# Kernel optimization log

Measured on AMD Instinct MI355X. Metric: run time of the kernel, lower is better.

## Reference

```python
import jax, jax.numpy as jnp
import numpy as np

H, HKV, D, HID = 32, 8, 128, 4096
EPS = 1e-6
ROPE_BASE = 10000.0
SCALE = D ** -0.5


def setup_inputs() -> dict:
    key = jax.random.key(0)
    ks = jax.random.split(key, 4)
    T = 2048
    x = jax.random.normal(ks[0], (T, HID), dtype=jnp.float32)
    w_qkv = jax.random.normal(ks[1], ((H + 2 * HKV) * D, HID), dtype=jnp.float32) * (HID ** -0.5)
    b_qkv = jax.random.normal(ks[2], ((H + 2 * HKV) * D,), dtype=jnp.float32) * 0.02
    q_norm_w = jnp.ones((D,), dtype=jnp.float32)
    k_norm_w = jnp.ones((D,), dtype=jnp.float32)
    w_o = jax.random.normal(ks[3], (HID, H * D), dtype=jnp.float32) * ((H * D) ** -0.5)
    return {"x": x, "w_qkv": w_qkv, "b_qkv": b_qkv, "q_norm_w": q_norm_w,
            "k_norm_w": k_norm_w, "w_o": w_o}


def _rms_norm(t, w):
    # per-head RMSNorm over the last (head_dim) axis
    var = jnp.mean(t * t, axis=-1, keepdims=True)
    return t * jax.lax.rsqrt(var + EPS) * w


def _rope(t, cos, sin):
    # neox-style half rotation; cos/sin: [T, D//2], t: [T, h, D]
    t1, t2 = jnp.split(t, 2, axis=-1)
    c = cos[:, None, :]
    s = sin[:, None, :]
    return jnp.concatenate([t1 * c - t2 * s, t2 * c + t1 * s], axis=-1)


def reference(x, w_qkv, b_qkv, q_norm_w, k_norm_w, w_o):
    T = x.shape[0]
    qkv = x @ w_qkv.T + b_qkv                      # [T, (H+2*HKV)*D]
    q, k, v = jnp.split(qkv, [H * D, (H + HKV) * D], axis=-1)
    q = q.reshape(T, H, D)
    k = k.reshape(T, HKV, D)
    v = v.reshape(T, HKV, D)

    # QK RMSNorm
    q = _rms_norm(q, q_norm_w)
    k = _rms_norm(k, k_norm_w)

    # rotary embedding, base 10000, full head_dim
    pos = jnp.arange(T, dtype=jnp.float32)
    inv_freq = 1.0 / (ROPE_BASE ** (jnp.arange(0, D, 2, dtype=jnp.float32) / D))
    freqs = pos[:, None] * inv_freq[None, :]        # [T, D//2]
    cos, sin = jnp.cos(freqs), jnp.sin(freqs)
    q = _rope(q, cos, sin)
    k = _rope(k, cos, sin)

    # GQA: kv_head_mapping = arange(HKV).repeat_interleave(H // HKV)
    groups = H // HKV
    k = jnp.repeat(k, groups, axis=1)               # [T, H, D]
    v = jnp.repeat(v, groups, axis=1)

    scores = jnp.einsum('thd,shd->hts', q, k) * SCALE   # [H, T, T]
    causal = jnp.tril(jnp.ones((T, T), dtype=bool))
    scores = jnp.where(causal[None], scores, jnp.finfo(scores.dtype).min)
    probs = jax.nn.softmax(scores, axis=-1)
    out = jnp.einsum('hts,shd->thd', probs, v)      # [T, H, D]
    return out.reshape(T, H * D) @ w_o.T            # [T, HID]
```

## Files before the change

kernel.cpp:

```cpp
#include <hip/hip_runtime.h>
#include <stdint.h>
#include <stddef.h>

typedef __bf16 bf16_t;
typedef __bf16 bf16x8 __attribute__((ext_vector_type(8)));
typedef float  f32x4  __attribute__((ext_vector_type(4)));
typedef float  f32x8  __attribute__((ext_vector_type(8)));

#define T_SEQ 2048
#define NH    32
#define NKV   8
#define DH    128
#define HIDN  4096
#define NQKV  6144
#define SCALE 0.08838834764831845f
#define MBOUND 11.5f

__device__ inline float b2f(bf16_t v) {
  uint32_t u = ((uint32_t)__builtin_bit_cast(uint16_t, v)) << 16;
  return __builtin_bit_cast(float, u);
}
__device__ inline bf16_t f2b(float f) { return (bf16_t)f; }
__device__ inline void gl_lds16(const void* g, void* l) {
  __builtin_amdgcn_global_load_lds(
      (__attribute__((address_space(1))) void*)g,
      (__attribute__((address_space(3))) void*)l, 16, 0, 0);
}
__device__ inline f32x4 mfma16(bf16x8 a, bf16x8 b, f32x4 c) {
  return __builtin_amdgcn_mfma_f32_16x16x32_bf16(a, b, c, 0, 0, 0);
}
__device__ inline void store_val(float* p, float v)  { *p = v; }
__device__ inline void store_val(bf16_t* p, float v) { *p = f2b(v); }

template <typename T> struct Pack8;
template <> struct Pack8<bf16_t> { using type = bf16x8; };
template <> struct Pack8<float>  { using type = f32x8; };
__device__ inline bf16x8 to_bf8(bf16x8 v) { return v; }
__device__ inline bf16x8 to_bf8(f32x8 v) {
  bf16x8 o;
#pragma unroll
  for (int e = 0; e < 8; ++e) o[e] = f2b(v[e]);
  return o;
}

template <bool BIAS, typename TA, typename TB, typename TOUT>
__global__ __launch_bounds__(256)
void gemm_bt(const TA* __restrict__ A, const TB* __restrict__ Bw,
             const float* __restrict__ bias, TOUT* __restrict__ C,
             int M, int N, int K) {
  __shared__ __align__(16) char smem[32768];
  char* sA = smem;
  char* sB = smem + 16384;
  const int tid  = threadIdx.x;
  const int lane = tid & 63, wave = tid >> 6;
  const int quad = lane >> 4, l16 = lane & 15;
  const int wm = wave >> 1, wn = wave & 1;
  const int m0 = blockIdx.y * 128, n0 = blockIdx.x * 128;

  typename Pack8<TA>::type rA[4];
  typename Pack8<TB>::type rB[4];
  auto load_tile = [&](int kb) {
#pragma unroll
    for (int i = 0; i < 4; ++i) {
      int p = i * 256 + tid;
      int row = p >> 3, gc = (p & 7) ^ (row & 7);
      rA[i] = *(const typename Pack8<TA>::type*)(A  + (size_t)(m0 + row) * K + kb + gc * 8);
      rB[i] = *(const typename Pack8<TB>::type*)(Bw + (size_t)(n0 + row) * K + kb + gc * 8);
    }
  };

  f32x4 acc[4][4] = {};
  const int kTiles = K >> 6;
  load_tile(0);

  for (int kt = 0; kt < kTiles; ++kt) {
    __syncthreads();
#pragma unroll
    for (int i = 0; i < 4; ++i) {
      int p = i * 256 + tid;
      *(bf16x8*)(sA + p * 16) = to_bf8(rA[i]);
      *(bf16x8*)(sB + p * 16) = to_bf8(rB[i]);
    }
    __syncthreads();
    if (kt + 1 < kTiles) load_tile((kt + 1) << 6);

#pragma unroll
    for (int ks = 0; ks < 2; ++ks) {
      bf16x8 af[4], bfr[4];
      const int c = ks * 4 + quad;
#pragma unroll
      for (int i = 0; i < 4; ++i) {
        int ra = wm * 64 + i * 16 + l16;
        af[i]  = *(const bf16x8*)(sA + ra * 128 + ((c ^ (ra & 7)) * 16));
        int rb = wn * 64 + i * 16 + l16;
        bfr[i] = *(const bf16x8*)(sB + rb * 128 + ((c ^ (rb & 7)) * 16));
      }
#pragma unroll
      for (int i = 0; i < 4; ++i)
#pragma unroll
        for (int j = 0; j < 4; ++j)
          acc[i][j] = mfma16(af[i], bfr[j], acc[i][j]);
    }
  }
#pragma unroll
  for (int i = 0; i < 4; ++i) {
    int mrow = m0 + wm * 64 + i * 16 + quad * 4;
#pragma unroll
    for (int j = 0; j < 4; ++j) {
      int ncol = n0 + wn * 64 + j * 16 + l16;
      float bv = BIAS ? bias[ncol] : 0.f;
#pragma unroll
      for (int r = 0; r < 4; ++r)
        store_val(&C[(size_t)(mrow + r) * N + ncol], acc[i][j][r] + bv);
    }
  }
}

__global__ __launch_bounds__(256)
void prep_kernel(const bf16_t* __restrict__ qkv, const float* __restrict__ qw,
                 const float* __restrict__ kw, bf16_t* __restrict__ Qp,
                 bf16_t* __restrict__ Kp, bf16_t* __restrict__ Vp) {
  const int id   = blockIdx.x * 4 + (threadIdx.x >> 6);
  const int lane = threadIdx.x & 63;
  const int t = id / 48, slot = id % 48;
  const bf16_t* src = qkv + (size_t)t * NQKV + slot * DH;
  float x1 = b2f(src[lane]), x2 = b2f(src[lane + 64]);
  float o1, o2;
  if (slot < 40) {
    float ssq = x1 * x1 + x2 * x2;
#pragma unroll
    for (int m = 1; m < 64; m <<= 1) ssq += __shfl_xor(ssq, m, 64);
    float rms = rsqrtf(ssq * (1.f / 128.f) + 1e-6f);
    const float* w = (slot < 32) ? qw : kw;
    float n1 = x1 * rms * w[lane];
    float n2 = x2 * rms * w[lane + 64];
    float inv = exp2f(-0.20762050593046014f * (float)lane);
    float ang = (float)t * inv;
    float cs = cosf(ang), sn = sinf(ang);
    o1 = n1 * cs - n2 * sn;
    o2 = n2 * cs + n1 * sn;
  } else { o1 = x1; o2 = x2; }
  bf16_t* dst;
  if (slot < 32)      dst = Qp + ((size_t)t * NH  + slot)        * DH;
  else if (slot < 40) dst = Kp + ((size_t)t * NKV + (slot - 32)) * DH;
  else                dst = Vp + ((size_t)t * NKV + (slot - 40)) * DH;
  dst[lane] = f2b(o1); dst[lane + 64] = f2b(o2);
}

__global__ __launch_bounds__(256)
void vtrans_kernel(const bf16_t* __restrict__ Vp, bf16_t* __restrict__ Vt) {
  __shared__ bf16_t tile[64 * 66];
  const int t0 = blockIdx.x * 64, d0 = blockIdx.y * 64, kvh = blockIdx.z;
  const int tid = threadIdx.x;
#pragma unroll
  for (int i = 0; i < 2; ++i) {
    int id = i * 256 + tid;
    int tr = id >> 3, dc = id & 7;
    bf16x8 v = *(const bf16x8*)(Vp + ((size_t)(t0 + tr) * NKV + kvh) * DH + d0 + dc * 8);
#pragma unroll
    for (int e = 0; e < 8; ++e) tile[tr * 66 + dc * 8 + e] = v[e];
  }
  __syncthreads();
#pragma unroll
  for (int i = 0; i < 2; ++i) {
    int id = i * 256 + tid;
    int dr = id >> 3, tc = id & 7;
    bf16x8 o;
#pragma unroll
    for (int e = 0; e < 8; ++e) o[e] = tile[(tc * 8 + e) * 66 + dr];
    *(bf16x8*)(Vt + ((size_t)kvh * DH + d0 + dr) * T_SEQ + t0 + tc * 8) = o;
  }
}

__global__ __launch_bounds__(256)
void attn_kernel(const bf16_t* __restrict__ Qp, const bf16_t* __restrict__ Kp,
                 const bf16_t* __restrict__ Vt, bf16_t* __restrict__ Out) {
  __shared__ __align__(16) char smem[73728];
  const int tid  = threadIdx.x;
  const int lane = tid & 63, wave = tid >> 6;
  const int quad = lane >> 4, l16 = lane & 15;
  const int b = blockIdx.x, h = blockIdx.y;
  const int qt_lo = b, qt_hi = 31 - b;
  const int kvh = h >> 2;
  char* sPw = smem + 65536 + wave * 2048;

  bf16x8 qf_lo[4], qf_hi[4];
  {
    const int row_lo = qt_lo * 64 + wave * 16 + l16;
    const int row_hi = qt_hi * 64 + wave * 16 + l16;
#pragma unroll
    for (int ks = 0; ks < 4; ++ks) {
      qf_lo[ks] = *(const bf16x8*)(Qp + ((size_t)row_lo * NH + h) * DH + ks * 32 + quad * 8);
      qf_hi[ks] = *(const bf16x8*)(Qp + ((size_t)row_hi * NH + h) * DH + ks * 32 + quad * 8);
    }
  }
  f32x4 acc_lo[8] = {}, acc_hi[8] = {};
  float l_lo[4] = {0.f, 0.f, 0.f, 0.f}, l_hi[4] = {0.f, 0.f, 0.f, 0.f};

  auto stage = [&](int kt) {
    char* sK = smem + (kt & 1) * 16384;
    char* sV = smem + 32768 + (kt & 1) * 16384;
    const int k0 = kt * 64;
#pragma unroll
    for (int i = 0; i < 4; ++i) {
      int p = i * 256 + tid;
      int row = p >> 4, gc = (p & 15) ^ (row & 15);
      gl_lds16(Kp + ((size_t)(k0 + row) * NKV + kvh) * DH + gc * 8, sK + p * 16);
    }
#pragma unroll
    for (int i = 0; i < 4; ++i) {
      int p = i * 256 + tid;
      int d = p >> 3, gc = (p & 7) ^ (d & 7);
      gl_lds16(Vt + ((size_t)kvh * DH + d) * T_SEQ + k0 + gc * 8, sV + p * 16);
    }
  };

  auto compute = [&](const bf16x8 (&qf)[4], f32x4 (&acc)[8], float (&lrow)[4],
                     int qt, int kt, char* sK, char* sVT) {
    f32x4 sfr[4] = {};
#pragma unroll
    for (int ks = 0; ks < 4; ++ks) {
      const int c = ks * 4 + quad;
#pragma unroll
      for (int j = 0; j < 4; ++j) {
        int row = j * 16 + l16;
        bf16x8 kf = *(const bf16x8*)(sK + row * 256 + ((c ^ (row & 15)) * 16));
        sfr[j] = mfma16(qf[ks], kf, sfr[j]);
      }
    }
    float sv[4][4];
    const bool diag = (kt == qt);
#pragma unroll
    for (int j = 0; j < 4; ++j)
#pragma unroll
      for (int r = 0; r < 4; ++r) {
        float e = __expf(fmaf(sfr[j][r], SCALE, -MBOUND));
        if (diag) {
          int qg = wave * 16 + quad * 4 + r;
          int kg = j * 16 + l16;
          if (kg > qg) e = 0.f;
        }
        sv[j][r] = e;
      }
#pragma unroll
    for (int r = 0; r < 4; ++r)
      lrow[r] += (sv[0][r] + sv[1][r]) + (sv[2][r] + sv[3][r]);
#pragma unroll
    for (int j = 0; j < 4; ++j)
#pragma unroll
      for (int r = 0; r < 4; ++r) {
        int prow = quad * 4 + r;
        int col  = j * 16 + l16;
        int c    = col >> 3;
        ((bf16_t*)(sPw + prow * 128 + ((c ^ (prow & 7)) * 16)))[col & 7] = f2b(sv[j][r]);
      }
    __asm__ volatile("" ::: "memory");
    bf16x8 pf[2];
#pragma unroll
    for (int ks2 = 0; ks2 < 2; ++ks2) {
      int c = ks2 * 4 + quad;
      pf[ks2] = *(const bf16x8*)(sPw + l16 * 128 + ((c ^ (l16 & 7)) * 16));
    }
    __asm__ volatile("" ::: "memory");
#pragma unroll
    for (int j2 = 0; j2 < 8; ++j2)
#pragma unroll
      for (int ks2 = 0; ks2 < 2; ++ks2) {
        int d = j2 * 16 + l16;
        int c = ks2 * 4 + quad;
        bf16x8 vf = *(const bf16x8*)(sVT + d * 128 + ((c ^ (d & 7)) * 16));
        acc[j2] = mfma16(pf[ks2], vf, acc[j2]);
      }
  };

  stage(0);
  for (int kt = 0; kt <= qt_hi; ++kt) {
    __syncthreads();
    if (kt < qt_hi) stage(kt + 1);
    char* sK  = smem + (kt & 1) * 16384;
    char* sVT = smem + 32768 + (kt & 1) * 16384;
    compute(qf_hi, acc_hi, l_hi, qt_hi, kt, sK, sVT);
    if (kt <= qt_lo)
      compute(qf_lo, acc_lo, l_lo, qt_lo, kt, sK, sVT);
  }

#pragma unroll
  for (int r = 0; r < 4; ++r) {
    float lh = l_hi[r], ll = l_lo[r];
#pragma unroll
    for (int m = 1; m < 16; m <<= 1) {
      lh += __shfl_xor(lh, m, 64);
      ll += __shfl_xor(ll, m, 64);
    }
    float inv_h = 1.f / lh, inv_l = 1.f / ll;
    int qg_h = qt_hi * 64 + wave * 16 + quad * 4 + r;
    int qg_l = qt_lo * 64 + wave * 16 + quad * 4 + r;
#pragma unroll
    for (int j2 = 0; j2 < 8; ++j2) {
      int d = j2 * 16 + l16;
      Out[(size_t)qg_h * (NH * DH) + h * DH + d] = f2b(acc_hi[j2][r] * inv_h);
      Out[(size_t)qg_l * (NH * DH) + h * DH + d] = f2b(acc_lo[j2][r] * inv_l);
    }
  }
}

extern "C" void kernel_launch(void* const* d_in, const int* in_sizes, int n_in,
                              void* d_out, int out_size, void* d_ws, size_t ws_size,
                              hipStream_t stream) {
  const float* x    = (const float*)d_in[0];
  const float* wqkv = (const float*)d_in[1];
  const float* bqkv = (const float*)d_in[2];
  const float* qnw  = (const float*)d_in[3];
  const float* knw  = (const float*)d_in[4];
  const float* wo   = (const float*)d_in[5];
  float* out = (float*)d_out;

  char* ws = (char*)d_ws;
  bf16_t* qkv = (bf16_t*)(ws);
  bf16_t* At  = (bf16_t*)(ws);
  bf16_t* Qp  = (bf16_t*)(ws + 33554432);
  bf16_t* Kp  = (bf16_t*)(ws + 50331648);
  bf16_t* Vp  = (bf16_t*)(ws + 54525952);
  bf16_t* Vt  = (bf16_t*)(ws + 58720256);

  gemm_bt<true, float, float, bf16_t><<<dim3(NQKV / 128, T_SEQ / 128), 256, 0, stream>>>(
      x, wqkv, bqkv, qkv, T_SEQ, NQKV, HIDN);
  prep_kernel<<<(T_SEQ * 48) / 4, 256, 0, stream>>>(qkv, qnw, knw, Qp, Kp, Vp);
  vtrans_kernel<<<dim3(T_SEQ / 64, DH / 64, NKV), 256, 0, stream>>>(Vp, Vt);
  attn_kernel<<<dim3(16, NH), 256, 0, stream>>>(Qp, Kp, Vt, At);
  gemm_bt<false, bf16_t, float, float><<<dim3(HIDN / 128, T_SEQ / 128), 256, 0, stream>>>(
      At, wo, nullptr, out, T_SEQ, HIDN, HIDN);
}
```

Measured before the change: 575.8 us.

## Pre-convert GEMM operands to bf16 and stream tiles via direct global-to-LDS loads

Adds a standalone fp32-to-bf16 conversion kernel that runs on x, w_qkv and w_o before the GEMMs. The GEMM kernel now takes bf16 operands only and fills LDS with global_load_lds instead of staging through registers. This removes in-kernel conversion and halves the bytes each GEMM reads. In exchange it adds three extra passes over the fp32 weights, and it drops the register prefetch, so global loads are no longer overlapped with MFMA work.

```diff
diff --git a/kernel.cpp b/kernel.cpp
--- a/kernel.cpp
+++ b/kernel.cpp
@@ -5,7 +5,6 @@
 typedef __bf16 bf16_t;
 typedef __bf16 bf16x8 __attribute__((ext_vector_type(8)));
 typedef float  f32x4  __attribute__((ext_vector_type(4)));
-typedef float  f32x8  __attribute__((ext_vector_type(8)));
 
 #define T_SEQ 2048
 #define NH    32
@@ -32,20 +31,20 @@
 __device__ inline void store_val(float* p, float v)  { *p = v; }
 __device__ inline void store_val(bf16_t* p, float v) { *p = f2b(v); }
 
-template <typename T> struct Pack8;
-template <> struct Pack8<bf16_t> { using type = bf16x8; };
-template <> struct Pack8<float>  { using type = f32x8; };
-__device__ inline bf16x8 to_bf8(bf16x8 v) { return v; }
-__device__ inline bf16x8 to_bf8(f32x8 v) {
+__global__ __launch_bounds__(256)
+void cvt_kernel(const float* __restrict__ in, bf16_t* __restrict__ out) {
+  size_t i = ((size_t)blockIdx.x * 256 + threadIdx.x) * 8;
+  f32x4 a = *(const f32x4*)(in + i);
+  f32x4 b = *(const f32x4*)(in + i + 4);
   bf16x8 o;
 #pragma unroll
-  for (int e = 0; e < 8; ++e) o[e] = f2b(v[e]);
-  return o;
-}
-
-template <bool BIAS, typename TA, typename TB, typename TOUT>
-__global__ __launch_bounds__(256)
-void gemm_bt(const TA* __restrict__ A, const TB* __restrict__ Bw,
+  for (int e = 0; e < 4; ++e) { o[e] = f2b(a[e]); o[e + 4] = f2b(b[e]); }
+  *(bf16x8*)(out + i) = o;
+}
+
+template <bool BIAS, typename TOUT>
+__global__ __launch_bounds__(256)
+void gemm_bt(const bf16_t* __restrict__ A, const bf16_t* __restrict__ Bw,
              const float* __restrict__ bias, TOUT* __restrict__ C,
              int M, int N, int K) {
   __shared__ __align__(16) char smem[32768];
@@ -57,32 +56,19 @@
   const int wm = wave >> 1, wn = wave & 1;
   const int m0 = blockIdx.y * 128, n0 = blockIdx.x * 128;
 
-  typename Pack8<TA>::type rA[4];
-  typename Pack8<TB>::type rB[4];
-  auto load_tile = [&](int kb) {
+  f32x4 acc[4][4] = {};
+  const int kTiles = K >> 6;
+
+  for (int kt = 0; kt < kTiles; ++kt) {
+    const int kb = kt << 6;
 #pragma unroll
     for (int i = 0; i < 4; ++i) {
       int p = i * 256 + tid;
       int row = p >> 3, gc = (p & 7) ^ (row & 7);
-      rA[i] = *(const typename Pack8<TA>::type*)(A  + (size_t)(m0 + row) * K + kb + gc * 8);
-      rB[i] = *(const typename Pack8<TB>::type*)(Bw + (size_t)(n0 + row) * K + kb + gc * 8);
-    }
-  };
-
-  f32x4 acc[4][4] = {};
-  const int kTiles = K >> 6;
-  load_tile(0);
-
-  for (int kt = 0; kt < kTiles; ++kt) {
+      gl_lds16(A  + (size_t)(m0 + row) * K + kb + gc * 8, sA + p * 16);
+      gl_lds16(Bw + (size_t)(n0 + row) * K + kb + gc * 8, sB + p * 16);
+    }
     __syncthreads();
-#pragma unroll
-    for (int i = 0; i < 4; ++i) {
-      int p = i * 256 + tid;
-      *(bf16x8*)(sA + p * 16) = to_bf8(rA[i]);
-      *(bf16x8*)(sB + p * 16) = to_bf8(rB[i]);
-    }
-    __syncthreads();
-    if (kt + 1 < kTiles) load_tile((kt + 1) << 6);
 
 #pragma unroll
     for (int ks = 0; ks < 2; ++ks) {
@@ -101,6 +87,7 @@
         for (int j = 0; j < 4; ++j)
           acc[i][j] = mfma16(af[i], bfr[j], acc[i][j]);
     }
+    __syncthreads();
   }
 #pragma unroll
   for (int i = 0; i < 4; ++i) {
@@ -316,18 +303,24 @@
   float* out = (float*)d_out;
 
   char* ws = (char*)d_ws;
-  bf16_t* qkv = (bf16_t*)(ws);
-  bf16_t* At  = (bf16_t*)(ws);
-  bf16_t* Qp  = (bf16_t*)(ws + 33554432);
-  bf16_t* Kp  = (bf16_t*)(ws + 50331648);
-  bf16_t* Vp  = (bf16_t*)(ws + 54525952);
-  bf16_t* Vt  = (bf16_t*)(ws + 58720256);
-
-  gemm_bt<true, float, float, bf16_t><<<dim3(NQKV / 128, T_SEQ / 128), 256, 0, stream>>>(
-      x, wqkv, bqkv, qkv, T_SEQ, NQKV, HIDN);
+  bf16_t* wqkvb = (bf16_t*)(ws);
+  bf16_t* xb    = (bf16_t*)(ws + 50331648);
+  bf16_t* qkv   = (bf16_t*)(ws + 67108864);
+  bf16_t* Qp    = (bf16_t*)(ws);
+  bf16_t* Kp    = (bf16_t*)(ws + 16777216);
+  bf16_t* Vp    = (bf16_t*)(ws + 20971520);
+  bf16_t* Vt    = (bf16_t*)(ws + 25165824);
+  bf16_t* wob   = (bf16_t*)(ws + 29360128);
+  bf16_t* At    = (bf16_t*)(ws + 67108864);
+
+  cvt_kernel<<<(T_SEQ * HIDN) / 2048, 256, 0, stream>>>(x, xb);
+  cvt_kernel<<<(NQKV * HIDN) / 2048, 256, 0, stream>>>(wqkv, wqkvb);
+  gemm_bt<true, bf16_t><<<dim3(NQKV / 128, T_SEQ / 128), 256, 0, stream>>>(
+      xb, wqkvb, bqkv, qkv, T_SEQ, NQKV, HIDN);
   prep_kernel<<<(T_SEQ * 48) / 4, 256, 0, stream>>>(qkv, qnw, knw, Qp, Kp, Vp);
   vtrans_kernel<<<dim3(T_SEQ / 64, DH / 64, NKV), 256, 0, stream>>>(Vp, Vt);
+  cvt_kernel<<<(HIDN * HIDN) / 2048, 256, 0, stream>>>(wo, wob);
   attn_kernel<<<dim3(16, NH), 256, 0, stream>>>(Qp, Kp, Vt, At);
-  gemm_bt<false, bf16_t, float, float><<<dim3(HIDN / 128, T_SEQ / 128), 256, 0, stream>>>(
-      At, wo, nullptr, out, T_SEQ, HIDN, HIDN);
-}
+  gemm_bt<false, float><<<dim3(HIDN / 128, T_SEQ / 128), 256, 0, stream>>>(
+      At, wob, nullptr, out, T_SEQ, HIDN, HIDN);
+}
```

After: 515.9 us. -10.4%, faster.
